# Performance work log

Hardware: AMD Instinct MI355X
Metric: run time of the kernel (lower is better)

## Reference

```python
import jax, jax.numpy as jnp
import numpy as np

EPS = 1e-16  # matches PyG softmax denominator epsilon


def setup_inputs() -> dict:
    key = jax.random.key(0)
    k1, k2, k3, k4 = jax.random.split(key, 4)
    N, F, G = 200000, 256, 1024
    x = jax.random.normal(k1, (N, F), dtype=jnp.float32)
    batch = jnp.sort(jax.random.randint(k2, (N,), 0, G, dtype=jnp.int64))
    Wg = jax.random.normal(k3, (F, 1), dtype=jnp.float32) / np.sqrt(F)
    bg = jnp.zeros((1,), dtype=jnp.float32)
    Wn = jax.random.normal(k4, (F, F), dtype=jnp.float32) / np.sqrt(F)
    bn = jnp.zeros((F,), dtype=jnp.float32)
    return {"x": x, "batch": batch, "size": G, "Wg": Wg, "bg": bg, "Wn": Wn, "bn": bn}


def reference(x, batch, size, Wg, bg, Wn, bn):
    # gate scores: [N, 1]
    gate = x @ Wg + bg
    # transformed features: [N, F]
    h = x @ Wn + bn
    # per-graph (segment) softmax over gate, numerically stable
    seg_max = jax.ops.segment_max(gate, batch, num_segments=size)  # [G, 1]
    e = jnp.exp(gate - seg_max[batch])                             # [N, 1]
    seg_sum = jax.ops.segment_sum(e, batch, num_segments=size)     # [G, 1]
    alpha = e / (seg_sum[batch] + EPS)                             # [N, 1]
    # weighted scatter-add: [G, F]
    out = jax.ops.segment_sum(alpha * h, batch, num_segments=size)
    return out
```

## Files before the change

### kernel.cpp

```cpp
#include <hip/hip_runtime.h>
#include <math.h>

#define FDIM 256
#define EPSF 1e-16f
#define K4_ROWS 2

__device__ __forceinline__ int lower_bound(const int* __restrict__ a, int n, int key) {
    int lo = 0, hi = n;
    while (lo < hi) {
        int mid = (lo + hi) >> 1;
        if (a[mid] < key) lo = mid + 1; else hi = mid;
    }
    return lo;
}

__global__ void __launch_bounds__(256) k_fused(const int* __restrict__ batch,
                                               const float* __restrict__ x,
                                               const float* __restrict__ Wg,
                                               float* __restrict__ y,
                                               float* __restrict__ sum_alpha, int N) {
    int g = blockIdx.x;
    __shared__ int s_range[2];
    __shared__ float s_s[8];
    __shared__ float s_acc[8][FDIM];
    if (threadIdx.x == 0) {
        s_range[0] = lower_bound(batch, N, g);
        s_range[1] = lower_bound(batch, N, g + 1);
    }
    __syncthreads();
    int start = s_range[0], end = s_range[1];
    int slot = threadIdx.x >> 6;
    int half = (threadIdx.x >> 5) & 1;
    int sub  = threadIdx.x & 31;

    const float4 wg1 = *reinterpret_cast<const float4*>(Wg + sub * 4);
    const float4 wg2 = *reinterpret_cast<const float4*>(Wg + 128 + sub * 4);

    float4 a1 = make_float4(0.f, 0.f, 0.f, 0.f);
    float4 a2 = make_float4(0.f, 0.f, 0.f, 0.f);
    float s = 0.f;

    for (int i = start + slot * 2; i < end; i += 8) {
        int r = i + half;
        bool valid = (r < end);
        float4 xv1 = make_float4(0.f, 0.f, 0.f, 0.f);
        float4 xv2 = make_float4(0.f, 0.f, 0.f, 0.f);
        if (valid) {
            const float* rp = x + (size_t)r * FDIM;
            xv1 = *reinterpret_cast<const float4*>(rp + sub * 4);
            xv2 = *reinterpret_cast<const float4*>(rp + 128 + sub * 4);
        }
        float d = xv1.x * wg1.x + xv1.y * wg1.y + xv1.z * wg1.z + xv1.w * wg1.w
                + xv2.x * wg2.x + xv2.y * wg2.y + xv2.z * wg2.z + xv2.w * wg2.w;
        #pragma unroll
        for (int off = 1; off < 32; off <<= 1) d += __shfl_xor(d, off, 64);
        float w = valid ? __expf(d) : 0.f;
        a1.x += w * xv1.x; a1.y += w * xv1.y; a1.z += w * xv1.z; a1.w += w * xv1.w;
        a2.x += w * xv2.x; a2.y += w * xv2.y; a2.z += w * xv2.z; a2.w += w * xv2.w;
        s += w;
    }

    int part = slot * 2 + half;
    *reinterpret_cast<float4*>(&s_acc[part][sub * 4]) = a1;
    *reinterpret_cast<float4*>(&s_acc[part][128 + sub * 4]) = a2;
    if (sub == 0) s_s[part] = s;
    __syncthreads();

    float tot = ((s_s[0] + s_s[1]) + (s_s[2] + s_s[3]))
              + ((s_s[4] + s_s[5]) + (s_s[6] + s_s[7]));
    float inv = 1.0f / (tot + EPSF);
    if (threadIdx.x == 0) sum_alpha[g] = tot * inv;

    int c = threadIdx.x;
    float v = 0.f;
    #pragma unroll
    for (int p = 0; p < 8; ++p) v += s_acc[p][c];
    y[(size_t)g * FDIM + c] = v * inv;
}

__global__ void __launch_bounds__(256) k4_out(const float* __restrict__ y,
                                              const float* __restrict__ Wn,
                                              const float* __restrict__ bn,
                                              const float* __restrict__ sum_alpha,
                                              float* __restrict__ out, int G) {
    int g0 = blockIdx.x * K4_ROWS;
    __shared__ float ys[K4_ROWS][FDIM];
    #pragma unroll
    for (int r = 0; r < K4_ROWS; ++r) {
        int g = g0 + r;
        ys[r][threadIdx.x] = (g < G) ? y[(size_t)g * FDIM + threadIdx.x] : 0.f;
    }
    __syncthreads();
    int f = threadIdx.x;
    float acc[K4_ROWS];
    #pragma unroll
    for (int r = 0; r < K4_ROWS; ++r) acc[r] = 0.f;
    #pragma unroll 8
    for (int k = 0; k < FDIM; ++k) {
        float w = Wn[k * FDIM + f];
        #pragma unroll
        for (int r = 0; r < K4_ROWS; ++r) acc[r] += ys[r][k] * w;
    }
    float b = bn[f];
    #pragma unroll
    for (int r = 0; r < K4_ROWS; ++r) {
        int g = g0 + r;
        if (g < G) out[(size_t)g * FDIM + f] = acc[r] + sum_alpha[g] * b;
    }
}

extern "C" void kernel_launch(void* const* d_in, const int* in_sizes, int n_in,
                              void* d_out, int out_size, void* d_ws, size_t ws_size,
                              hipStream_t stream) {
    const float* x     = (const float*)d_in[0];
    const int*   batch = (const int*)d_in[1];
    const float* Wg    = (const float*)d_in[3];
    const float* Wn    = (const float*)d_in[5];
    const float* bn    = (const float*)d_in[6];
    float* out = (float*)d_out;

    int N = in_sizes[1];
    int G = out_size / FDIM;

    float* sum_alpha = (float*)d_ws;
    float* y = sum_alpha + G;

    k_fused<<<G, 256, 0, stream>>>(batch, x, Wg, y, sum_alpha, N);
    k4_out<<<(G + K4_ROWS - 1) / K4_ROWS, 256, 0, stream>>>(y, Wn, bn, sum_alpha, out, G);
}
```

Baseline: 53.36 us.

## Split each graph across two blocks and use 16-lane row groups

Each graph segment is now split in half and handled by two blocks, doubling the grid so more CUs stay busy. Each wave processes four rows at a time using 16-lane groups with four float4 loads per lane, which cuts shuffle depth and removes the per-row validity masking. Partial weighted sums and exp-sums are written per half, and the output kernel merges the two halves, normalizes, and applies the bias scale. In exchange it doubles the partial-buffer traffic and the binary searches, and it still applies exp without subtracting the segment max, so large gate scores could overflow.

```diff
diff --git a/kernel.cpp b/kernel.cpp
--- a/kernel.cpp
+++ b/kernel.cpp
@@ -14,98 +14,118 @@
     return lo;
 }
 
+__device__ __forceinline__ float dot4(float4 a, float4 b) {
+    return a.x * b.x + a.y * b.y + a.z * b.z + a.w * b.w;
+}
+
 __global__ void __launch_bounds__(256) k_fused(const int* __restrict__ batch,
                                                const float* __restrict__ x,
                                                const float* __restrict__ Wg,
-                                               float* __restrict__ y,
-                                               float* __restrict__ sum_alpha, int N) {
-    int g = blockIdx.x;
+                                               float* __restrict__ yp,
+                                               float* __restrict__ sp, int N) {
+    int b = blockIdx.x;
+    int g = b >> 1, half = b & 1;
     __shared__ int s_range[2];
-    __shared__ float s_s[8];
-    __shared__ float s_acc[8][FDIM];
+    __shared__ float s_s[16];
+    __shared__ float s_acc[16][FDIM];
     if (threadIdx.x == 0) {
-        s_range[0] = lower_bound(batch, N, g);
-        s_range[1] = lower_bound(batch, N, g + 1);
+        int s0 = lower_bound(batch, N, g);
+        int e0 = lower_bound(batch, N, g + 1);
+        int mid = s0 + ((e0 - s0) >> 1);
+        s_range[0] = half ? mid : s0;
+        s_range[1] = half ? e0 : mid;
     }
     __syncthreads();
-    int start = s_range[0], end = s_range[1];
-    int slot = threadIdx.x >> 6;
-    int half = (threadIdx.x >> 5) & 1;
-    int sub  = threadIdx.x & 31;
+    int rs = s_range[0], re = s_range[1];
+    int wave = threadIdx.x >> 6;
+    int group = (threadIdx.x >> 4) & 3;
+    int l16 = threadIdx.x & 15;
+    int part = (wave << 2) | group;
 
-    const float4 wg1 = *reinterpret_cast<const float4*>(Wg + sub * 4);
-    const float4 wg2 = *reinterpret_cast<const float4*>(Wg + 128 + sub * 4);
+    const float4 wg0 = *reinterpret_cast<const float4*>(Wg +   0 + l16 * 4);
+    const float4 wg1 = *reinterpret_cast<const float4*>(Wg +  64 + l16 * 4);
+    const float4 wg2 = *reinterpret_cast<const float4*>(Wg + 128 + l16 * 4);
+    const float4 wg3 = *reinterpret_cast<const float4*>(Wg + 192 + l16 * 4);
 
-    float4 a1 = make_float4(0.f, 0.f, 0.f, 0.f);
-    float4 a2 = make_float4(0.f, 0.f, 0.f, 0.f);
+    float4 a0 = make_float4(0.f, 0.f, 0.f, 0.f);
+    float4 a1 = a0, a2 = a0, a3 = a0;
     float s = 0.f;
 
-    for (int i = start + slot * 2; i < end; i += 8) {
-        int r = i + half;
-        bool valid = (r < end);
-        float4 xv1 = make_float4(0.f, 0.f, 0.f, 0.f);
-        float4 xv2 = make_float4(0.f, 0.f, 0.f, 0.f);
-        if (valid) {
-            const float* rp = x + (size_t)r * FDIM;
-            xv1 = *reinterpret_cast<const float4*>(rp + sub * 4);
-            xv2 = *reinterpret_cast<const float4*>(rp + 128 + sub * 4);
-        }
-        float d = xv1.x * wg1.x + xv1.y * wg1.y + xv1.z * wg1.z + xv1.w * wg1.w
-                + xv2.x * wg2.x + xv2.y * wg2.y + xv2.z * wg2.z + xv2.w * wg2.w;
+    for (int r = rs + part; r < re; r += 16) {
+        const float* rp = x + (size_t)r * FDIM;
+        float4 x0 = *reinterpret_cast<const float4*>(rp +   0 + l16 * 4);
+        float4 x1 = *reinterpret_cast<const float4*>(rp +  64 + l16 * 4);
+        float4 x2 = *reinterpret_cast<const float4*>(rp + 128 + l16 * 4);
+        float4 x3 = *reinterpret_cast<const float4*>(rp + 192 + l16 * 4);
+        float d = dot4(x0, wg0) + dot4(x1, wg1) + dot4(x2, wg2) + dot4(x3, wg3);
         #pragma unroll
-        for (int off = 1; off < 32; off <<= 1) d += __shfl_xor(d, off, 64);
-        float w = valid ? __expf(d) : 0.f;
-        a1.x += w * xv1.x; a1.y += w * xv1.y; a1.z += w * xv1.z; a1.w += w * xv1.w;
-        a2.x += w * xv2.x; a2.y += w * xv2.y; a2.z += w * xv2.z; a2.w += w * xv2.w;
+        for (int off = 1; off < 16; off <<= 1) d += __shfl_xor(d, off, 64);
+        float w = __expf(d);
+        a0.x += w * x0.x; a0.y += w * x0.y; a0.z += w * x0.z; a0.w += w * x0.w;
+        a1.x += w * x1.x; a1.y += w * x1.y; a1.z += w * x1.z; a1.w += w * x1.w;
+        a2.x += w * x2.x; a2.y += w * x2.y; a2.z += w * x2.z; a2.w += w * x2.w;
+        a3.x += w * x3.x; a3.y += w * x3.y; a3.z += w * x3.z; a3.w += w * x3.w;
         s += w;
     }
 
-    int part = slot * 2 + half;
-    *reinterpret_cast<float4*>(&s_acc[part][sub * 4]) = a1;
-    *reinterpret_cast<float4*>(&s_acc[part][128 + sub * 4]) = a2;
-    if (sub == 0) s_s[part] = s;
+    *reinterpret_cast<float4*>(&s_acc[part][  0 + l16 * 4]) = a0;
+    *reinterpret_cast<float4*>(&s_acc[part][ 64 + l16 * 4]) = a1;
+    *reinterpret_cast<float4*>(&s_acc[part][128 + l16 * 4]) = a2;
+    *reinterpret_cast<float4*>(&s_acc[part][192 + l16 * 4]) = a3;
+    if (l16 == 0) s_s[part] = s;
     __syncthreads();
-
-    float tot = ((s_s[0] + s_s[1]) + (s_s[2] + s_s[3]))
-              + ((s_s[4] + s_s[5]) + (s_s[6] + s_s[7]));
-    float inv = 1.0f / (tot + EPSF);
-    if (threadIdx.x == 0) sum_alpha[g] = tot * inv;
 
     int c = threadIdx.x;
     float v = 0.f;
     #pragma unroll
-    for (int p = 0; p < 8; ++p) v += s_acc[p][c];
-    y[(size_t)g * FDIM + c] = v * inv;
+    for (int p = 0; p < 16; ++p) v += s_acc[p][c];
+    yp[(size_t)b * FDIM + c] = v;
+    if (threadIdx.x == 0) {
+        float t = 0.f;
+        #pragma unroll
+        for (int p = 0; p < 16; ++p) t += s_s[p];
+        sp[b] = t;
+    }
 }
 
-__global__ void __launch_bounds__(256) k4_out(const float* __restrict__ y,
+__global__ void __launch_bounds__(256) k4_out(const float* __restrict__ yp,
+                                              const float* __restrict__ sp,
                                               const float* __restrict__ Wn,
                                               const float* __restrict__ bn,
-                                              const float* __restrict__ sum_alpha,
                                               float* __restrict__ out, int G) {
     int g0 = blockIdx.x * K4_ROWS;
     __shared__ float ys[K4_ROWS][FDIM];
+    __shared__ float s_alpha[K4_ROWS];
+    int c = threadIdx.x;
     #pragma unroll
     for (int r = 0; r < K4_ROWS; ++r) {
         int g = g0 + r;
-        ys[r][threadIdx.x] = (g < G) ? y[(size_t)g * FDIM + threadIdx.x] : 0.f;
+        if (g < G) {
+            float sg = sp[2 * g] + sp[2 * g + 1];
+            float inv = 1.0f / (sg + EPSF);
+            ys[r][c] = (yp[(size_t)(2 * g) * FDIM + c] +
+                        yp[(size_t)(2 * g + 1) * FDIM + c]) * inv;
+            if (c == 0) s_alpha[r] = sg * inv;
+        } else {
+            ys[r][c] = 0.f;
+            if (c == 0) s_alpha[r] = 0.f;
+        }
     }
     __syncthreads();
-    int f = threadIdx.x;
     float acc[K4_ROWS];
     #pragma unroll
     for (int r = 0; r < K4_ROWS; ++r) acc[r] = 0.f;
     #pragma unroll 8
     for (int k = 0; k < FDIM; ++k) {
-        float w = Wn[k * FDIM + f];
+        float w = Wn[k * FDIM + c];
         #pragma unroll
         for (int r = 0; r < K4_ROWS; ++r) acc[r] += ys[r][k] * w;
     }
-    float b = bn[f];
+    float bv = bn[c];
     #pragma unroll
     for (int r = 0; r < K4_ROWS; ++r) {
         int g = g0 + r;
-        if (g < G) out[(size_t)g * FDIM + f] = acc[r] + sum_alpha[g] * b;
+        if (g < G) out[(size_t)g * FDIM + c] = acc[r] + s_alpha[r] * bv;
     }
 }
 
@@ -122,9 +142,9 @@
     int N = in_sizes[1];
     int G = out_size / FDIM;
 
-    float* sum_alpha = (float*)d_ws;
-    float* y = sum_alpha + G;
+    float* sp = (float*)d_ws;
+    float* yp = sp + 2 * G;
 
-    k_fused<<<G, 256, 0, stream>>>(batch, x, Wg, y, sum_alpha, N);
-    k4_out<<<(G + K4_ROWS - 1) / K4_ROWS, 256, 0, stream>>>(y, Wn, bn, sum_alpha, out, G);
+    k_fused<<<2 * G, 256, 0, stream>>>(batch, x, Wg, yp, sp, N);
+    k4_out<<<(G + K4_ROWS - 1) / K4_ROWS, 256, 0, stream>>>(yp, sp, Wn, bn, out, G);
 }
```

Measured after the change: 58.51 us. 9.7% more time.
